# Performance work log

Measured on AMD Instinct MI355X. Metric: run time of the kernel, lower is better.

The kernel has to match this reference:

```python
import jax, jax.numpy as jnp
import numpy as np

D_MODEL = 1024
NUM_HEADS = 16
HEAD_DIM = D_MODEL // NUM_HEADS
ROPE_THETA = 10000.0


def apply_rope(x):
    # x: (B, H, S, d_k) interleaved-pair RoPE, angles pos / theta^(2i/d_k)
    S, d_k = x.shape[-2], x.shape[-1]
    inv_freq = ROPE_THETA ** (jnp.arange(0, d_k, 2, dtype=jnp.float32) / d_k)
    ang = jnp.arange(S, dtype=jnp.float32)[:, None] / inv_freq[None, :]  # (S, d_k/2)
    cos, sin = jnp.cos(ang), jnp.sin(ang)
    xp = x.reshape(x.shape[:-1] + (d_k // 2, 2))
    x0, x1 = xp[..., 0], xp[..., 1]
    out = jnp.stack([x0 * cos - x1 * sin, x0 * sin + x1 * cos], axis=-1)
    return out.reshape(x.shape)


def setup_inputs() -> dict:
    key = jax.random.key(0)
    k1, k2, k3 = jax.random.split(key, 3)
    B, S = 2, 2048
    std = 2.0 / (D_MODEL + 3 * D_MODEL)
    std_o = 2.0 / (D_MODEL + D_MODEL)
    return {
        "x": jax.random.normal(k1, (B, S, D_MODEL), dtype=jnp.float32),
        "W_qkv": jax.random.normal(k2, (3 * D_MODEL, D_MODEL), dtype=jnp.float32) * std,
        "W_o": jax.random.normal(k3, (D_MODEL, D_MODEL), dtype=jnp.float32) * std_o,
    }


def reference(x, W_qkv, W_o):
    B, S, d_model = x.shape
    H, d_k = NUM_HEADS, HEAD_DIM
    qkv = jnp.einsum('bsi,oi->bso', x, W_qkv)  # (B, S, 3*d_model)
    Q, K, V = jnp.split(qkv, 3, axis=-1)
    # (B, S, d_model) -> (B, H, S, d_k)
    def to_heads(t):
        return t.reshape(B, S, H, d_k).transpose(0, 2, 1, 3)
    Q, K, V = to_heads(Q), to_heads(K), to_heads(V)
    Q, K = apply_rope(Q), apply_rope(K)
    scores = jnp.einsum('bhqd,bhkd->bhqk', Q, K) / jnp.sqrt(jnp.float32(d_k))
    causal = jnp.tril(jnp.ones((S, S), dtype=bool))
    scores = jnp.where(causal, scores, -jnp.inf)
    attn = jax.nn.softmax(scores, axis=-1)
    out = jnp.einsum('bhqk,bhkd->bhqd', attn, V)
    out = out.transpose(0, 2, 1, 3).reshape(B, S, d_model)
    return jnp.einsum('bsi,oi->bso', out, W_o)
```

## Files before the change

### kernel.cpp

```cpp
#include <hip/hip_runtime.h>
#include <math.h>

#define kB 2
#define kS 2048
#define kD 1024
#define kH 16
#define kDk 64
#define kM (kB * kS)
#define kNT (kD / 64)
#define kLog2Theta 13.287712379549449
#define C_SCALE 0.18033688011112042f

typedef __attribute__((ext_vector_type(4))) float f32x4;
typedef __attribute__((ext_vector_type(16))) float f32x16;
typedef __attribute__((ext_vector_type(8))) __bf16 bf16x8;

__device__ __forceinline__ ushort f2bf(float f) {
  uint u = __float_as_uint(f);
  return (ushort)((u + 0x7fffu + ((u >> 16) & 1u)) >> 16);
}
__device__ __forceinline__ uint cvt_pk_bf16(float lo, float hi) {
  uint r;
  asm("v_cvt_pk_bf16_f32 %0, %1, %2" : "=v"(r) : "v"(lo), "v"(hi));
  return r;
}

typedef __attribute__((address_space(1))) void gvoid;
typedef __attribute__((address_space(3))) void lvoid;
__device__ __forceinline__ void load_lds16(const void* g, void* l) {
  __builtin_amdgcn_global_load_lds((gvoid*)g, (lvoid*)l, 16, 0, 0);
}

__global__ __launch_bounds__(256) void rope_table_kernel(float2* __restrict__ tab) {
  const int i = blockIdx.x * 256 + threadIdx.x;
  const int s = i >> 5, p = i & 31;
  const double ang = (double)s * exp2(-(double)p * (kLog2Theta / 32.0));
  tab[i] = make_float2((float)cos(ang), (float)sin(ang));
}

__global__ __launch_bounds__(256) void cast_all_kernel(
    const float* __restrict__ x, const float* __restrict__ wq,
    const float* __restrict__ wo, ushort* __restrict__ xb,
    ushort* __restrict__ wqb, ushort* __restrict__ wob) {
  const int i = blockIdx.x * 256 + threadIdx.x;
  const float* src;
  ushort* dst;
  int off;
  if (i < 1048576) {
    src = x; dst = xb; off = i;
  } else if (i < 1048576 + 786432) {
    src = wq; dst = wqb; off = i - 1048576;
  } else {
    src = wo; dst = wob; off = i - 1835008;
  }
  const float4 v = reinterpret_cast<const float4*>(src)[off];
  ushort4 o;
  o.x = f2bf(v.x); o.y = f2bf(v.y); o.z = f2bf(v.z); o.w = f2bf(v.w);
  reinterpret_cast<ushort4*>(dst)[off] = o;
}

__global__ __launch_bounds__(256) void vtrans_kernel(
    const ushort* __restrict__ v, ushort* __restrict__ vt) {
  __shared__ ushort T[64 * 66];
  const int bh = blockIdx.y, st = blockIdx.x;
  const int tid = threadIdx.x;
  const ushort* vp = v + ((size_t)bh * kS + st * 64) * kDk;
#pragma unroll
  for (int u = 0; u < 2; ++u) {
    const int idx = u * 256 + tid;
    const int r = idx >> 3, c = (idx & 7) << 3;
    const uint4 d4 = *reinterpret_cast<const uint4*>(&vp[r * 64 + c]);
    uint* dst = reinterpret_cast<uint*>(&T[r * 66 + c]);
    dst[0] = d4.x; dst[1] = d4.y; dst[2] = d4.z; dst[3] = d4.w;
  }
  __syncthreads();
  const int d = tid >> 2, seg = tid & 3;
  ushort tmp[16];
#pragma unroll
  for (int j = 0; j < 16; ++j) tmp[j] = T[(seg * 16 + j) * 66 + d];
  ushort* dst = vt + ((size_t)bh * kDk + d) * kS + st * 64 + seg * 16;
  *reinterpret_cast<uint4*>(dst) = *reinterpret_cast<uint4*>(tmp);
  *reinterpret_cast<uint4*>(dst + 8) = *reinterpret_cast<uint4*>(tmp + 8);
}

__device__ __forceinline__ void gemm128_mainloop(
    const ushort* __restrict__ A, const ushort* __restrict__ B,
    int m0, int n0, int tid,
    ushort* As0, ushort* Bs0, ushort* As1, ushort* Bs1,
    f32x4 (&acc)[4][4]) {
  const int lane = tid & 63;
  const int wid = tid >> 6;
  const int wm = (wid >> 1) << 6, wn = (wid & 1) << 6;
  const int fr = lane & 15, fq = lane >> 4;

  auto stage = [&](int k0, ushort* Ad, ushort* Bd) {
#pragma unroll
    for (int u = 0; u < 4; ++u) {
      const int c = u * 256 + tid;
      const int r = c >> 3, sl = c & 7;
      const int col = k0 + ((sl ^ (r & 7)) << 3);
      load_lds16(&A[(size_t)(m0 + r) * kD + col], &Ad[c << 3]);
      load_lds16(&B[(size_t)(n0 + r) * kD + col], &Bd[c << 3]);
    }
  };
  auto rdfrag = [&](const ushort* S, int row, int kk) -> bf16x8 {
    const int off = ((kk << 5) + (fq << 3)) ^ ((row & 7) << 3);
    return *reinterpret_cast<const bf16x8*>(&S[(row << 6) + off]);
  };

  stage(0, As0, Bs0);

  auto tile = [&](const ushort* cA, const ushort* cB, ushort* nA, ushort* nB,
                  bool pf, int k0n) {
    asm volatile("s_waitcnt vmcnt(0)" ::: "memory");
    __builtin_amdgcn_s_barrier();
    __builtin_amdgcn_sched_barrier(0);
    bf16x8 af[2][4], bf_[2][4];
#pragma unroll
    for (int kk = 0; kk < 2; ++kk)
#pragma unroll
      for (int f = 0; f < 4; ++f) {
        af[kk][f]  = rdfrag(cA, wm + f * 16 + fr, kk);
        bf_[kk][f] = rdfrag(cB, wn + f * 16 + fr, kk);
      }
    if (pf) stage(k0n, nA, nB);
    asm volatile("s_waitcnt lgkmcnt(0)" ::: "memory");
    __builtin_amdgcn_sched_barrier(0);
    __builtin_amdgcn_s_setprio(1);
#pragma unroll
    for (int kk = 0; kk < 2; ++kk)
#pragma unroll
      for (int i = 0; i < 4; ++i)
#pragma unroll
        for (int j = 0; j < 4; ++j)
          acc[i][j] = __builtin_amdgcn_mfma_f32_16x16x32_bf16(
              af[kk][i], bf_[kk][j], acc[i][j], 0, 0, 0);
    __builtin_amdgcn_s_setprio(0);
  };

  for (int t = 0; t < kNT; t += 2) {
    tile(As0, Bs0, As1, Bs1, true, (t + 1) << 6);
    tile(As1, Bs1, As0, Bs0, t + 2 < kNT, (t + 2) << 6);
  }
}

__global__ __launch_bounds__(256) void qkv_mfma_kernel(
    const ushort* __restrict__ xb, const ushort* __restrict__ wqb,
    const float2* __restrict__ tab,
    ushort* __restrict__ q, ushort* __restrict__ k, ushort* __restrict__ v) {
  __shared__ ushort As0[128 * 64], Bs0[128 * 64];
  __shared__ ushort As1[128 * 64], Bs1[128 * 64];
  const int tid = threadIdx.x;
  const int m0 = blockIdx.y << 7, n0 = blockIdx.x << 7;
  f32x4 acc[4][4];
#pragma unroll
  for (int i = 0; i < 4; ++i)
#pragma unroll
    for (int j = 0; j < 4; ++j) acc[i][j] = {0.f, 0.f, 0.f, 0.f};

  gemm128_mainloop(xb, wqb, m0, n0, tid, As0, Bs0, As1, Bs1, acc);

  const int lane = tid & 63;
  const int wid = tid >> 6;
  const int wm = (wid >> 1) << 6, wn = (wid & 1) << 6;
  const int fr = lane & 15, fq = lane >> 4;
  const int t = n0 >> 10;
  ushort* dst = (t == 0) ? q : (t == 1) ? k : v;

#pragma unroll
  for (int i = 0; i < 4; ++i) {
    const int mbase = m0 + wm + i * 16 + fq * 4;
#pragma unroll
    for (int j = 0; j < 4; ++j) {
      const int n = n0 + wn + j * 16 + fr;
      const int h = (n >> 6) & 15, d = n & 63;
#pragma unroll
      for (int r = 0; r < 4; ++r) {
        const int m = mbase + r;
        const int b = m >> 11, s = m & (kS - 1);
        float val = acc[i][j][r];
        if (t < 2) {
          const float2 cs = tab[(s << 5) + (d >> 1)];
          const float partner = __shfl_xor(val, 1);
          val = (d & 1) ? (partner * cs.y + val * cs.x)
                        : (val * cs.x - partner * cs.y);
        }
        if (t == 0) val *= C_SCALE;
        dst[(((size_t)((b << 4) + h) << 11) + s) * kDk + d] = f2bf(val);
      }
    }
  }
}

__global__ __launch_bounds__(256) void proj_mfma_kernel(
    const ushort* __restrict__ ab, const ushort* __restrict__ wob,
    float* __restrict__ out) {
  __shared__ ushort As0[128 * 64], Bs0[128 * 64];
  __shared__ ushort As1[128 * 64], Bs1[128 * 64];
  const int tid = threadIdx.x;
  const int m0 = blockIdx.y << 7, n0 = blockIdx.x << 7;
  f32x4 acc[4][4];
#pragma unroll
  for (int i = 0; i < 4; ++i)
#pragma unroll
    for (int j = 0; j < 4; ++j) acc[i][j] = {0.f, 0.f, 0.f, 0.f};

  gemm128_mainloop(ab, wob, m0, n0, tid, As0, Bs0, As1, Bs1, acc);

  const int lane = tid & 63;
  const int wid = tid >> 6;
  const int wm = (wid >> 1) << 6, wn = (wid & 1) << 6;
  const int fr = lane & 15, fq = lane >> 4;
#pragma unroll
  for (int i = 0; i < 4; ++i)
#pragma unroll
    for (int j = 0; j < 4; ++j)
#pragma unroll
      for (int r = 0; r < 4; ++r)
        out[(size_t)(m0 + wm + i * 16 + fq * 4 + r) * kD + n0 + wn + j * 16 + fr] =
            acc[i][j][r];
}

__global__ __launch_bounds__(256) void attn_mfma_kernel(
    const ushort* __restrict__ q, const ushort* __restrict__ k,
    const ushort* __restrict__ vt, ushort* __restrict__ ob) {
  __shared__ ushort smem[32768];
  const int tid = threadIdx.x;
  const int lane = tid & 63;
  const int wq = tid >> 6;
  const int l5 = lane >> 5;
  const int ln = lane & 31;
  const int swz = (ln & 7) << 4;

  const int idx = blockIdx.x;
  const int grp = idx >> 5, bh = idx & 31;
  const int qi = (grp < 8) ? (15 - grp) : (grp - 8);
  const int qb = qi << 7;
  const int nt = qi + 1;

  const ushort* qp = q + (size_t)bh * kS * kDk;
  const ushort* kp = k + (size_t)bh * kS * kDk;
  const ushort* vp = vt + (size_t)bh * kDk * kS;

  bf16x8 bq[4];
#pragma unroll
  for (int kk = 0; kk < 4; ++kk)
    bq[kk] = *reinterpret_cast<const bf16x8*>(
        &qp[(size_t)(qb + wq * 32 + ln) * kDk + kk * 16 + l5 * 8]);

  f32x16 acc_o[2];
#pragma unroll
  for (int db = 0; db < 2; ++db)
#pragma unroll
    for (int r = 0; r < 16; ++r) acc_o[db][r] = 0.f;
  float l_run = 0.f;

  auto stage = [&](int kt, int buf) {
    ushort* Kd = smem + buf * 16384;
    ushort* Vd = Kd + 8192;
#pragma unroll
    for (int u = 0; u < 4; ++u) {
      const int c = u * 256 + tid;
      {
        const int r = c >> 3, sl = c & 7;
        load_lds16(&kp[(size_t)(kt * 128 + r) * kDk + ((sl ^ (r & 7)) << 3)],
                   &Kd[c << 3]);
      }
      {
        const int r = c >> 4, sl = c & 15;
        load_lds16(&vp[(size_t)r * kS + kt * 128 + ((sl ^ (r & 7)) << 3)],
                   &Vd[c << 3]);
      }
    }
  };

  stage(0, 0);

  for (int kt = 0; kt < nt; ++kt) {
    const int cur = kt & 1;
    __syncthreads();
    if (kt + 1 < nt) stage(kt + 1, cur ^ 1);

    const char* KsB = reinterpret_cast<const char*>(smem + cur * 16384);
    const char* VtsB = KsB + 16384;

    f32x16 accs[4];
    __builtin_amdgcn_s_setprio(1);
#pragma unroll
    for (int cb = 0; cb < 4; ++cb) {
#pragma unroll
      for (int r = 0; r < 16; ++r) accs[cb][r] = 0.f;
#pragma unroll
      for (int kk = 0; kk < 4; ++kk) {
        const bf16x8 av = *reinterpret_cast<const bf16x8*>(
            KsB + (cb * 32 + ln) * 128 + ((kk * 32 + l5 * 16) ^ swz));
        accs[cb] = __builtin_amdgcn_mfma_f32_32x32x16_bf16(av, bq[kk], accs[cb], 0, 0, 0);
      }
    }
    __builtin_amdgcn_s_setprio(0);

    if (kt == qi) {
      const int lim = (wq << 5) + ln;
#pragma unroll
      for (int cb = 0; cb < 4; ++cb)
#pragma unroll
        for (int r = 0; r < 16; ++r) {
          const int key = cb * 32 + (r & 3) + 8 * (r >> 2) + 4 * l5;
          if (key > lim) accs[cb][r] = -INFINITY;
        }
    }

    uint c8[4][8];
    float lsum = 0.f;
#pragma unroll
    for (int cb = 0; cb < 4; ++cb) {
      float s0 = 0.f, s1 = 0.f, s2 = 0.f, s3 = 0.f;
      float p[16];
#pragma unroll
      for (int r = 0; r < 16; ++r) {
        p[r] = exp2f(accs[cb][r]);
        if ((r & 3) == 0) s0 += p[r];
        else if ((r & 3) == 1) s1 += p[r];
        else if ((r & 3) == 2) s2 += p[r];
        else s3 += p[r];
      }
      lsum += (s0 + s1) + (s2 + s3);
#pragma unroll
      for (int t = 0; t < 8; ++t)
        c8[cb][t] = cvt_pk_bf16(p[2 * t], p[2 * t + 1]);
    }
    l_run += lsum;

    __builtin_amdgcn_s_setprio(1);
#pragma unroll
    for (int kb = 0; kb < 8; ++kb) {
      const int cb = kb >> 1, base = (kb & 1) * 4;
      const uint a0 = c8[cb][base + 0], a1 = c8[cb][base + 1];
      const uint b0 = c8[cb][base + 2], b1 = c8[cb][base + 3];
      const uint sa0 = (uint)__shfl_xor((int)a0, 32);
      const uint sa1 = (uint)__shfl_xor((int)a1, 32);
      const uint sb0 = (uint)__shfl_xor((int)b0, 32);
      const uint sb1 = (uint)__shfl_xor((int)b1, 32);
      uint4 dw;
      dw.x = l5 ? sb0 : a0;
      dw.y = l5 ? sb1 : a1;
      dw.z = l5 ? b0 : sa0;
      dw.w = l5 ? b1 : sa1;
      const bf16x8 pa = *reinterpret_cast<const bf16x8*>(&dw);
#pragma unroll
      for (int db = 0; db < 2; ++db) {
        const bf16x8 av = *reinterpret_cast<const bf16x8*>(
            VtsB + (db * 32 + ln) * 256 + ((kb * 32 + l5 * 16) ^ swz));
        acc_o[db] = __builtin_amdgcn_mfma_f32_32x32x16_bf16(av, pa, acc_o[db], 0, 0, 0);
      }
    }
    __builtin_amdgcn_s_setprio(0);
  }

  const float l_tot = l_run + __shfl_xor(l_run, 32);
  const float linv = 1.f / l_tot;

  __syncthreads();
  char* OsB = reinterpret_cast<char*>(smem);
  const int orow = wq * 32 + ln;
#pragma unroll
  for (int db = 0; db < 2; ++db)
#pragma unroll
    for (int t = 0; t < 8; ++t) {
      const int reg = 2 * t;
      const int d = db * 32 + (reg & 3) + 8 * (reg >> 2) + 4 * l5;
      const uint pk2 = cvt_pk_bf16(acc_o[db][reg] * linv, acc_o[db][reg + 1] * linv);
      *reinterpret_cast<uint*>(OsB + orow * 128 + ((d * 2) ^ swz)) = pk2;
    }
  __syncthreads();
  const int b = bh >> 4, h = bh & 15;
  const int qrw = tid >> 1, half = tid & 1;
  ushort* orow_g = ob + ((size_t)(b * kS + qb + qrw)) * kD + h * kDk + half * 32;
#pragma unroll
  for (int sl = 0; sl < 4; ++sl) {
    const uint4 vdat = *reinterpret_cast<const uint4*>(
        OsB + qrw * 128 + ((half * 64 + sl * 16) ^ ((qrw & 7) << 4)));
    *reinterpret_cast<uint4*>(orow_g + sl * 8) = vdat;
  }
}

extern "C" void kernel_launch(void* const* d_in, const int* in_sizes, int n_in,
                              void* d_out, int out_size, void* d_ws,
                              size_t ws_size, hipStream_t stream) {
  const float* x = (const float*)d_in[0];
  const float* wqkv = (const float*)d_in[1];
  const float* wo = (const float*)d_in[2];
  float* out = (float*)d_out;
  char* w = (char*)d_ws;
  const size_t MB = 1024 * 1024;
  ushort* qb  = (ushort*)(w + 0 * MB);
  ushort* kb  = (ushort*)(w + 8 * MB);
  ushort* vb  = (ushort*)(w + 16 * MB);
  ushort* xb  = (ushort*)(w + 24 * MB);
  ushort* wqb = (ushort*)(w + 32 * MB);
  ushort* wob = (ushort*)(w + 38 * MB);
  float2* tab = (float2*)(w + 40 * MB);
  ushort* vtb = (ushort*)(w + 41 * MB);
  ushort* attnb = xb;

  hipLaunchKernelGGL(rope_table_kernel, dim3(256), dim3(256), 0, stream, tab);
  hipLaunchKernelGGL(cast_all_kernel, dim3(8192), dim3(256), 0, stream,
                     x, wqkv, wo, xb, wqb, wob);
  hipLaunchKernelGGL(qkv_mfma_kernel, dim3(3 * kD / 128, kM / 128), dim3(256),
                     0, stream, xb, wqb, tab, qb, kb, vb);
  hipLaunchKernelGGL(vtrans_kernel, dim3(kS / 64, kB * kH), dim3(256), 0,
                     stream, vb, vtb);
  hipLaunchKernelGGL(attn_mfma_kernel, dim3(512), dim3(256), 0, stream,
                     qb, kb, vtb, attnb);
  hipLaunchKernelGGL(proj_mfma_kernel, dim3(kD / 128, kM / 128), dim3(256), 0,
                     stream, attnb, wob, out);
}
```

Before: 149.2 us.

## Fuse V transpose into QKV GEMM, enlarge QKV tiles, add XCD-aware block mapping

The QKV GEMM now uses 256x256 tiles with 512 threads and writes V directly in transposed layout, so the separate vtrans kernel and its extra V round-trip are gone. The QKV, projection and attention kernels remap block IDs so that blocks sharing operands land on the same XCD, which should improve L2 reuse. The larger QKV tile raises arithmetic intensity but uses 128 KB of LDS and 128 accumulator registers per thread. That limits occupancy to one block per CU and launches only 192 blocks, which may underfill the device.

```diff
diff --git a/kernel.cpp b/kernel.cpp
--- a/kernel.cpp
+++ b/kernel.cpp
@@ -59,48 +59,146 @@
   reinterpret_cast<ushort4*>(dst)[off] = o;
 }
 
-__global__ __launch_bounds__(256) void vtrans_kernel(
-    const ushort* __restrict__ v, ushort* __restrict__ vt) {
-  __shared__ ushort T[64 * 66];
-  const int bh = blockIdx.y, st = blockIdx.x;
+__global__ __launch_bounds__(512) void qkv_mfma_kernel(
+    const ushort* __restrict__ xb, const ushort* __restrict__ wqb,
+    const float2* __restrict__ tab,
+    ushort* __restrict__ q, ushort* __restrict__ k, ushort* __restrict__ vt) {
+  __shared__ ushort As0[256 * 64], Bs0[256 * 64];
+  __shared__ ushort As1[256 * 64], Bs1[256 * 64];
   const int tid = threadIdx.x;
-  const ushort* vp = v + ((size_t)bh * kS + st * 64) * kDk;
-#pragma unroll
-  for (int u = 0; u < 2; ++u) {
-    const int idx = u * 256 + tid;
-    const int r = idx >> 3, c = (idx & 7) << 3;
-    const uint4 d4 = *reinterpret_cast<const uint4*>(&vp[r * 64 + c]);
-    uint* dst = reinterpret_cast<uint*>(&T[r * 66 + c]);
-    dst[0] = d4.x; dst[1] = d4.y; dst[2] = d4.z; dst[3] = d4.w;
-  }
-  __syncthreads();
-  const int d = tid >> 2, seg = tid & 3;
-  ushort tmp[16];
-#pragma unroll
-  for (int j = 0; j < 16; ++j) tmp[j] = T[(seg * 16 + j) * 66 + d];
-  ushort* dst = vt + ((size_t)bh * kDk + d) * kS + st * 64 + seg * 16;
-  *reinterpret_cast<uint4*>(dst) = *reinterpret_cast<uint4*>(tmp);
-  *reinterpret_cast<uint4*>(dst + 8) = *reinterpret_cast<uint4*>(tmp + 8);
-}
-
-__device__ __forceinline__ void gemm128_mainloop(
-    const ushort* __restrict__ A, const ushort* __restrict__ B,
-    int m0, int n0, int tid,
-    ushort* As0, ushort* Bs0, ushort* As1, ushort* Bs1,
-    f32x4 (&acc)[4][4]) {
+  const int lane = tid & 63;
+  const int wid = tid >> 6;
+  const int wmi = wid >> 2, wni = wid & 3;
+  const int fr = lane & 15, fq = lane >> 4;
+
+  const int bid = blockIdx.x;
+  const int xcd = bid & 7, li = bid >> 3;
+  const int mt = ((xcd >> 1) << 2) + (li & 3);
+  const int ntl = (xcd & 1) * 6 + (li >> 2);
+  const int m0 = mt << 8, n0 = ntl << 8;
+
+  f32x4 acc[8][4];
+#pragma unroll
+  for (int i = 0; i < 8; ++i)
+#pragma unroll
+    for (int j = 0; j < 4; ++j) acc[i][j] = {0.f, 0.f, 0.f, 0.f};
+
+  auto stage = [&](int k0, ushort* Ad, ushort* Bd) {
+#pragma unroll
+    for (int u = 0; u < 4; ++u) {
+      const int c = u * 512 + tid;
+      const int r = c >> 3, sl = c & 7;
+      const int col = k0 + ((sl ^ (r & 7)) << 3);
+      load_lds16(&xb[(size_t)(m0 + r) * kD + col], &Ad[c << 3]);
+      load_lds16(&wqb[(size_t)(n0 + r) * kD + col], &Bd[c << 3]);
+    }
+  };
+  auto rdfrag = [&](const ushort* S, int row, int kk) -> bf16x8 {
+    const int off = ((kk << 5) + (fq << 3)) ^ ((row & 7) << 3);
+    return *reinterpret_cast<const bf16x8*>(&S[(row << 6) + off]);
+  };
+
+  stage(0, As0, Bs0);
+
+  auto tile = [&](const ushort* cA, const ushort* cB, ushort* nA, ushort* nB,
+                  bool pf, int k0n) {
+    asm volatile("s_waitcnt vmcnt(0)" ::: "memory");
+    __builtin_amdgcn_s_barrier();
+    __builtin_amdgcn_sched_barrier(0);
+#pragma unroll
+    for (int kk = 0; kk < 2; ++kk) {
+      bf16x8 af[8], bf_[4];
+#pragma unroll
+      for (int f = 0; f < 8; ++f)
+        af[f] = rdfrag(cA, (wmi << 7) + f * 16 + fr, kk);
+#pragma unroll
+      for (int f = 0; f < 4; ++f)
+        bf_[f] = rdfrag(cB, (wni << 6) + f * 16 + fr, kk);
+      if (kk == 0 && pf) stage(k0n, nA, nB);
+      asm volatile("s_waitcnt lgkmcnt(0)" ::: "memory");
+      __builtin_amdgcn_sched_barrier(0);
+      __builtin_amdgcn_s_setprio(1);
+#pragma unroll
+      for (int i = 0; i < 8; ++i)
+#pragma unroll
+        for (int j = 0; j < 4; ++j)
+          acc[i][j] = __builtin_amdgcn_mfma_f32_16x16x32_bf16(
+              af[i], bf_[j], acc[i][j], 0, 0, 0);
+      __builtin_amdgcn_s_setprio(0);
+    }
+  };
+
+  for (int t = 0; t < kNT; t += 2) {
+    tile(As0, Bs0, As1, Bs1, true, (t + 1) << 6);
+    tile(As1, Bs1, As0, Bs0, t + 2 < kNT, (t + 2) << 6);
+  }
+
+  const int tsel = n0 >> 10;
+#pragma unroll
+  for (int i = 0; i < 8; ++i) {
+    const int mbase = m0 + (wmi << 7) + i * 16 + fq * 4;
+    const int b = mbase >> 11, sbase = mbase & (kS - 1);
+#pragma unroll
+    for (int j = 0; j < 4; ++j) {
+      const int n = n0 + (wni << 6) + j * 16 + fr;
+      const int h = (n >> 6) & 15, d = n & 63;
+      if (tsel == 2) {
+        ushort4 o;
+        o.x = f2bf(acc[i][j][0]);
+        o.y = f2bf(acc[i][j][1]);
+        o.z = f2bf(acc[i][j][2]);
+        o.w = f2bf(acc[i][j][3]);
+        *reinterpret_cast<ushort4*>(
+            &vt[(((size_t)((b << 4) + h) << 6) + d) * kS + sbase]) = o;
+      } else {
+        ushort* dst = (tsel == 0) ? q : k;
+#pragma unroll
+        for (int r = 0; r < 4; ++r) {
+          const int s = sbase + r;
+          float val = acc[i][j][r];
+          const float2 cs = tab[(s << 5) + (d >> 1)];
+          const float partner = __shfl_xor(val, 1);
+          val = (d & 1) ? (partner * cs.y + val * cs.x)
+                        : (val * cs.x - partner * cs.y);
+          if (tsel == 0) val *= C_SCALE;
+          dst[(((size_t)((b << 4) + h) << 11) + s) * kDk + d] = f2bf(val);
+        }
+      }
+    }
+  }
+}
+
+__global__ __launch_bounds__(256) void proj_mfma_kernel(
+    const ushort* __restrict__ ab, const ushort* __restrict__ wob,
+    float* __restrict__ out) {
+  __shared__ ushort As0[128 * 64], Bs0[128 * 64];
+  __shared__ ushort As1[128 * 64], Bs1[128 * 64];
+  const int tid = threadIdx.x;
   const int lane = tid & 63;
   const int wid = tid >> 6;
   const int wm = (wid >> 1) << 6, wn = (wid & 1) << 6;
   const int fr = lane & 15, fq = lane >> 4;
 
+  const int bid = blockIdx.x;
+  const int xcd = bid & 7, li = bid >> 3;
+  const int mt = ((xcd >> 1) << 3) + (li & 7);
+  const int ntl = ((xcd & 1) << 2) + (li >> 3);
+  const int m0 = mt << 7, n0 = ntl << 7;
+
+  f32x4 acc[4][4];
+#pragma unroll
+  for (int i = 0; i < 4; ++i)
+#pragma unroll
+    for (int j = 0; j < 4; ++j) acc[i][j] = {0.f, 0.f, 0.f, 0.f};
+
   auto stage = [&](int k0, ushort* Ad, ushort* Bd) {
 #pragma unroll
     for (int u = 0; u < 4; ++u) {
       const int c = u * 256 + tid;
       const int r = c >> 3, sl = c & 7;
       const int col = k0 + ((sl ^ (r & 7)) << 3);
-      load_lds16(&A[(size_t)(m0 + r) * kD + col], &Ad[c << 3]);
-      load_lds16(&B[(size_t)(n0 + r) * kD + col], &Bd[c << 3]);
+      load_lds16(&ab[(size_t)(m0 + r) * kD + col], &Ad[c << 3]);
+      load_lds16(&wob[(size_t)(n0 + r) * kD + col], &Bd[c << 3]);
     }
   };
   auto rdfrag = [&](const ushort* S, int row, int kk) -> bf16x8 {
@@ -142,75 +240,7 @@
     tile(As0, Bs0, As1, Bs1, true, (t + 1) << 6);
     tile(As1, Bs1, As0, Bs0, t + 2 < kNT, (t + 2) << 6);
   }
-}
-
-__global__ __launch_bounds__(256) void qkv_mfma_kernel(
-    const ushort* __restrict__ xb, const ushort* __restrict__ wqb,
-    const float2* __restrict__ tab,
-    ushort* __restrict__ q, ushort* __restrict__ k, ushort* __restrict__ v) {
-  __shared__ ushort As0[128 * 64], Bs0[128 * 64];
-  __shared__ ushort As1[128 * 64], Bs1[128 * 64];
-  const int tid = threadIdx.x;
-  const int m0 = blockIdx.y << 7, n0 = blockIdx.x << 7;
-  f32x4 acc[4][4];
-#pragma unroll
-  for (int i = 0; i < 4; ++i)
-#pragma unroll
-    for (int j = 0; j < 4; ++j) acc[i][j] = {0.f, 0.f, 0.f, 0.f};
-
-  gemm128_mainloop(xb, wqb, m0, n0, tid, As0, Bs0, As1, Bs1, acc);
-
-  const int lane = tid & 63;
-  const int wid = tid >> 6;
-  const int wm = (wid >> 1) << 6, wn = (wid & 1) << 6;
-  const int fr = lane & 15, fq = lane >> 4;
-  const int t = n0 >> 10;
-  ushort* dst = (t == 0) ? q : (t == 1) ? k : v;
-
-#pragma unroll
-  for (int i = 0; i < 4; ++i) {
-    const int mbase = m0 + wm + i * 16 + fq * 4;
-#pragma unroll
-    for (int j = 0; j < 4; ++j) {
-      const int n = n0 + wn + j * 16 + fr;
-      const int h = (n >> 6) & 15, d = n & 63;
-#pragma unroll
-      for (int r = 0; r < 4; ++r) {
-        const int m = mbase + r;
-        const int b = m >> 11, s = m & (kS - 1);
-        float val = acc[i][j][r];
-        if (t < 2) {
-          const float2 cs = tab[(s << 5) + (d >> 1)];
-          const float partner = __shfl_xor(val, 1);
-          val = (d & 1) ? (partner * cs.y + val * cs.x)
-                        : (val * cs.x - partner * cs.y);
-        }
-        if (t == 0) val *= C_SCALE;
-        dst[(((size_t)((b << 4) + h) << 11) + s) * kDk + d] = f2bf(val);
-      }
-    }
-  }
-}
-
-__global__ __launch_bounds__(256) void proj_mfma_kernel(
-    const ushort* __restrict__ ab, const ushort* __restrict__ wob,
-    float* __restrict__ out) {
-  __shared__ ushort As0[128 * 64], Bs0[128 * 64];
-  __shared__ ushort As1[128 * 64], Bs1[128 * 64];
-  const int tid = threadIdx.x;
-  const int m0 = blockIdx.y << 7, n0 = blockIdx.x << 7;
-  f32x4 acc[4][4];
-#pragma unroll
-  for (int i = 0; i < 4; ++i)
-#pragma unroll
-    for (int j = 0; j < 4; ++j) acc[i][j] = {0.f, 0.f, 0.f, 0.f};
-
-  gemm128_mainloop(ab, wob, m0, n0, tid, As0, Bs0, As1, Bs1, acc);
-
-  const int lane = tid & 63;
-  const int wid = tid >> 6;
-  const int wm = (wid >> 1) << 6, wn = (wid & 1) << 6;
-  const int fr = lane & 15, fq = lane >> 4;
+
 #pragma unroll
   for (int i = 0; i < 4; ++i)
 #pragma unroll
@@ -232,8 +262,10 @@
   const int ln = lane & 31;
   const int swz = (ln & 7) << 4;
 
-  const int idx = blockIdx.x;
-  const int grp = idx >> 5, bh = idx & 31;
+  const int bidx = blockIdx.x;
+  const int xcd = bidx & 7, li = bidx >> 3;
+  const int bh = (xcd << 2) + (li & 3);
+  const int grp = li >> 2;
   const int qi = (grp < 8) ? (15 - grp) : (grp - 8);
   const int qb = qi << 7;
   const int nt = qi + 1;
@@ -395,23 +427,20 @@
   const size_t MB = 1024 * 1024;
   ushort* qb  = (ushort*)(w + 0 * MB);
   ushort* kb  = (ushort*)(w + 8 * MB);
-  ushort* vb  = (ushort*)(w + 16 * MB);
+  ushort* vtb = (ushort*)(w + 16 * MB);
   ushort* xb  = (ushort*)(w + 24 * MB);
   ushort* wqb = (ushort*)(w + 32 * MB);
   ushort* wob = (ushort*)(w + 38 * MB);
   float2* tab = (float2*)(w + 40 * MB);
-  ushort* vtb = (ushort*)(w + 41 * MB);
   ushort* attnb = xb;
 
   hipLaunchKernelGGL(rope_table_kernel, dim3(256), dim3(256), 0, stream, tab);
   hipLaunchKernelGGL(cast_all_kernel, dim3(8192), dim3(256), 0, stream,
                      x, wqkv, wo, xb, wqb, wob);
-  hipLaunchKernelGGL(qkv_mfma_kernel, dim3(3 * kD / 128, kM / 128), dim3(256),
-                     0, stream, xb, wqb, tab, qb, kb, vb);
-  hipLaunchKernelGGL(vtrans_kernel, dim3(kS / 64, kB * kH), dim3(256), 0,
-                     stream, vb, vtb);
+  hipLaunchKernelGGL(qkv_mfma_kernel, dim3(192), dim3(512), 0, stream,
+                     xb, wqb, tab, qb, kb, vtb);
   hipLaunchKernelGGL(attn_mfma_kernel, dim3(512), dim3(256), 0, stream,
                      qb, kb, vtb, attnb);
-  hipLaunchKernelGGL(proj_mfma_kernel, dim3(kD / 128, kM / 128), dim3(256), 0,
-                     stream, attnb, wob, out);
-}
+  hipLaunchKernelGGL(proj_mfma_kernel, dim3(256), dim3(256), 0, stream,
+                     attnb, wob, out);
+}
```

New measurement: 146.8 us. About the same (-1.6%).
